# Kernel optimization log

Measured on AMD Instinct MI355X. Metric: run time of the kernel, lower is better.

Reference implementation:

```python
import jax, jax.numpy as jnp
import numpy as np

D_MODEL = 1024
NUM_HEADS = 16
HEAD_DIM = D_MODEL // NUM_HEADS


def setup_inputs() -> dict:
    key = jax.random.key(0)
    ks = jax.random.split(key, 11)
    B, S = 4, 2048
    scale = 1.0 / np.sqrt(D_MODEL)
    inp = {
        'q': jax.random.normal(ks[0], (B, S, D_MODEL), jnp.float32),
        'k': jax.random.normal(ks[1], (B, S, D_MODEL), jnp.float32),
        'v': jax.random.normal(ks[2], (B, S, D_MODEL), jnp.float32),
        'Wq': jax.random.normal(ks[3], (D_MODEL, D_MODEL), jnp.float32) * scale,
        'bq': jnp.zeros((D_MODEL,), jnp.float32),
        'Wk': jax.random.normal(ks[4], (D_MODEL, D_MODEL), jnp.float32) * scale,
        'bk': jnp.zeros((D_MODEL,), jnp.float32),
        'Wv': jax.random.normal(ks[5], (D_MODEL, D_MODEL), jnp.float32) * scale,
        'bv': jnp.zeros((D_MODEL,), jnp.float32),
        'Wo': jax.random.normal(ks[6], (D_MODEL, D_MODEL), jnp.float32) * scale,
        'bo': jnp.zeros((D_MODEL,), jnp.float32),
    }
    return inp


def _split_heads(x):
    B, S, _ = x.shape
    return x.reshape(B, S, NUM_HEADS, HEAD_DIM).transpose(0, 2, 1, 3)  # [B,H,S,Dh]


def reference(q, k, v, Wq, bq, Wk, bk, Wv, bv, Wo, bo):
    Q = _split_heads(q @ Wq.T + bq)
    K = _split_heads(k @ Wk.T + bk)
    V = _split_heads(v @ Wv.T + bv)
    scores = jnp.einsum('bhqd,bhkd->bhqk', Q, K) / jnp.sqrt(jnp.float32(HEAD_DIM))
    attn = jax.nn.softmax(scores, axis=-1)
    out = jnp.einsum('bhqk,bhkd->bhqd', attn, V)  # [B,H,S,Dh]
    B, _, S, _ = out.shape
    out = out.transpose(0, 2, 1, 3).reshape(B, S, D_MODEL)
    return out @ Wo.T + bo
```

## Files before the change

kernel.cpp:

```cpp
#include <hip/hip_runtime.h>
#include <hip/hip_bf16.h>

#define DMODEL 1024
#define NHEADS 16
#define HDIM 64

typedef __bf16 bf16_t;
typedef __bf16 bf16x8 __attribute__((ext_vector_type(8)));
typedef float  f32x4  __attribute__((ext_vector_type(4)));
typedef float  f32x16 __attribute__((ext_vector_type(16)));

__device__ __forceinline__ bf16_t f2bf(float f) {
    unsigned int u = __builtin_bit_cast(unsigned int, f);
    u += 0x7FFF + ((u >> 16) & 1);
    unsigned short h = (unsigned short)(u >> 16);
    return __builtin_bit_cast(bf16_t, h);
}

__device__ __forceinline__ unsigned cvt_pk_bf16(float lo, float hi) {
    unsigned r;
    asm("v_cvt_pk_bf16_f32 %0, %1, %2" : "=v"(r) : "v"(lo), "v"(hi));
    return r;
}

__device__ __forceinline__ void gld_lds16(const bf16_t* g, bf16_t* l) {
    __builtin_amdgcn_global_load_lds(
        (const __attribute__((address_space(1))) unsigned int*)g,
        (__attribute__((address_space(3))) unsigned int*)l, 16, 0, 0);
}

__global__ __launch_bounds__(256) void cast4(const float* __restrict__ s0,
                                             const float* __restrict__ s1,
                                             const float* __restrict__ s2,
                                             const float* __restrict__ s3,
                                             bf16_t* __restrict__ d, int n) {
    int y = blockIdx.y;
    const float* s = (y == 0) ? s0 : (y == 1) ? s1 : (y == 2) ? s2 : s3;
    bf16_t* dst = d + (size_t)y * n;
    int i = blockIdx.x * blockDim.x + threadIdx.x;
    int stride = gridDim.x * blockDim.x;
    for (int idx = i * 4; idx < n; idx += stride * 4) {
        float4 v = *reinterpret_cast<const float4*>(s + idx);
        uint2 u;
        u.x = cvt_pk_bf16(v.x, v.y);
        u.y = cvt_pk_bf16(v.z, v.w);
        *reinterpret_cast<uint2*>(dst + idx) = u;
    }
}

__global__ __launch_bounds__(256) void cast3(const float* __restrict__ q,
                                             const float* __restrict__ k,
                                             const float* __restrict__ v,
                                             bf16_t* __restrict__ qb,
                                             bf16_t* __restrict__ kb,
                                             bf16_t* __restrict__ vb, int n) {
    int z = blockIdx.y;
    const float* s = (z == 0) ? q : (z == 1) ? k : v;
    bf16_t* d = (z == 0) ? qb : (z == 1) ? kb : vb;
    int i = blockIdx.x * blockDim.x + threadIdx.x;
    int stride = gridDim.x * blockDim.x;
    for (int idx = i * 4; idx < n; idx += stride * 4) {
        float4 vv = *reinterpret_cast<const float4*>(s + idx);
        uint2 u;
        u.x = cvt_pk_bf16(vv.x, vv.y);
        u.y = cvt_pk_bf16(vv.z, vv.w);
        *reinterpret_cast<uint2*>(d + idx) = u;
    }
}

__global__ __launch_bounds__(256) void gemm_qkv(const bf16_t* __restrict__ qb,
                                                const bf16_t* __restrict__ kb,
                                                const bf16_t* __restrict__ vb,
                                                const bf16_t* __restrict__ Wall,
                                                const float* __restrict__ bq,
                                                const float* __restrict__ bk,
                                                const float* __restrict__ bv,
                                                bf16_t* __restrict__ Qp,
                                                bf16_t* __restrict__ Kp,
                                                bf16_t* __restrict__ VtG,
                                                int M, float qscale, int S) {
    __shared__ bf16_t Asmem[2][128 * 32];
    __shared__ bf16_t Bsmem[2][128 * 32];
    const int K = DMODEL, N = DMODEL;
    const int z = blockIdx.z;
    const bf16_t* Ab = (z == 0) ? qb : (z == 1) ? kb : vb;
    const bf16_t* W = Wall + (size_t)z * DMODEL * DMODEL;
    const float* bias = (z == 0) ? bq : (z == 1) ? bk : bv;
    const float scale = (z == 0) ? qscale : 1.0f;

    const int m0 = blockIdx.x * 128;
    const int n0 = blockIdx.y * 128;
    const int tid = threadIdx.x;
    const int wave = tid >> 6, lane = tid & 63;
    const int wm = wave >> 1, wn = wave & 1;
    const int lr = lane & 15, lg = lane >> 4;
    const int srow = lane >> 2, scol = (lane & 3) * 8;

    f32x4 acc[4][4];
#pragma unroll
    for (int mi = 0; mi < 4; ++mi)
#pragma unroll
        for (int ni = 0; ni < 4; ++ni) acc[mi][ni] = (f32x4){0.f, 0.f, 0.f, 0.f};

#pragma unroll
    for (int i = 0; i < 2; ++i) {
        int c = wave * 2 + i;
        gld_lds16(Ab + (size_t)(m0 + c * 16 + srow) * K + scol, &Asmem[0][c * 512]);
        gld_lds16(W + (size_t)(n0 + c * 16 + srow) * K + scol, &Bsmem[0][c * 512]);
    }
    asm volatile("s_waitcnt vmcnt(0)" ::: "memory");
    __syncthreads();

    const int nk = K / 32;
    for (int t = 0; t < nk; ++t) {
        const int cur = t & 1, nxt = cur ^ 1;
        const int ktn = (t + 1) * 32;
        if (t + 1 < nk) {
#pragma unroll
            for (int i = 0; i < 2; ++i) {
                int c = wave * 2 + i;
                gld_lds16(Ab + (size_t)(m0 + c * 16 + srow) * K + ktn + scol, &Asmem[nxt][c * 512]);
                gld_lds16(W + (size_t)(n0 + c * 16 + srow) * K + ktn + scol, &Bsmem[nxt][c * 512]);
            }
        }
        bf16x8 af[4], bfr[4];
#pragma unroll
        for (int mi = 0; mi < 4; ++mi)
            af[mi] = *reinterpret_cast<const bf16x8*>(&Asmem[cur][(wm * 64 + mi * 16 + lr) * 32 + lg * 8]);
#pragma unroll
        for (int ni = 0; ni < 4; ++ni)
            bfr[ni] = *reinterpret_cast<const bf16x8*>(&Bsmem[cur][(wn * 64 + ni * 16 + lr) * 32 + lg * 8]);
#pragma unroll
        for (int mi = 0; mi < 4; ++mi)
#pragma unroll
            for (int ni = 0; ni < 4; ++ni)
                acc[mi][ni] = __builtin_amdgcn_mfma_f32_16x16x32_bf16(af[mi], bfr[ni], acc[mi][ni], 0, 0, 0);
        asm volatile("s_waitcnt vmcnt(0)" ::: "memory");
        __syncthreads();
    }

#pragma unroll
    for (int mi = 0; mi < 4; ++mi) {
        int row = m0 + wm * 64 + mi * 16 + lg * 4;
#pragma unroll
        for (int ni = 0; ni < 4; ++ni) {
            int col = n0 + wn * 64 + ni * 16 + lr;
            float bv_ = bias[col];
            if (z == 2) {
                union { bf16_t b[4]; uint2 u; } pq;
#pragma unroll
                for (int r = 0; r < 4; ++r) pq.b[r] = f2bf(acc[mi][ni][r] + bv_);
                int b_ = row / S, s_ = row % S;
                size_t addr = (((size_t)b_ * NHEADS + (col >> 6)) * HDIM + (col & 63)) * (size_t)S + s_;
                *reinterpret_cast<uint2*>(VtG + addr) = pq.u;
            } else {
                bf16_t* Cb = (z == 0) ? Qp : Kp;
#pragma unroll
                for (int r = 0; r < 4; ++r)
                    Cb[(size_t)(row + r) * N + col] = f2bf((acc[mi][ni][r] + bv_) * scale);
            }
        }
    }
}

__global__ __launch_bounds__(256) void gemm_out(const bf16_t* __restrict__ Ab,
                                                const bf16_t* __restrict__ W,
                                                const float* __restrict__ bias,
                                                float* __restrict__ Cout,
                                                int M, int N, int K) {
    __shared__ bf16_t Asmem[2][128 * 32];
    __shared__ bf16_t Bsmem[2][128 * 32];
    const int m0 = blockIdx.x * 128;
    const int n0 = blockIdx.y * 128;
    const int tid = threadIdx.x;
    const int wave = tid >> 6, lane = tid & 63;
    const int wm = wave >> 1, wn = wave & 1;
    const int lr = lane & 15, lg = lane >> 4;
    const int srow = lane >> 2, scol = (lane & 3) * 8;

    f32x4 acc[4][4];
#pragma unroll
    for (int mi = 0; mi < 4; ++mi)
#pragma unroll
        for (int ni = 0; ni < 4; ++ni) acc[mi][ni] = (f32x4){0.f, 0.f, 0.f, 0.f};

#pragma unroll
    for (int i = 0; i < 2; ++i) {
        int c = wave * 2 + i;
        gld_lds16(Ab + (size_t)(m0 + c * 16 + srow) * K + scol, &Asmem[0][c * 512]);
        gld_lds16(W + (size_t)(n0 + c * 16 + srow) * K + scol, &Bsmem[0][c * 512]);
    }
    asm volatile("s_waitcnt vmcnt(0)" ::: "memory");
    __syncthreads();

    const int nk = K / 32;
    for (int t = 0; t < nk; ++t) {
        const int cur = t & 1, nxt = cur ^ 1;
        const int ktn = (t + 1) * 32;
        if (t + 1 < nk) {
#pragma unroll
            for (int i = 0; i < 2; ++i) {
                int c = wave * 2 + i;
                gld_lds16(Ab + (size_t)(m0 + c * 16 + srow) * K + ktn + scol, &Asmem[nxt][c * 512]);
                gld_lds16(W + (size_t)(n0 + c * 16 + srow) * K + ktn + scol, &Bsmem[nxt][c * 512]);
            }
        }
        bf16x8 af[4], bfr[4];
#pragma unroll
        for (int mi = 0; mi < 4; ++mi)
            af[mi] = *reinterpret_cast<const bf16x8*>(&Asmem[cur][(wm * 64 + mi * 16 + lr) * 32 + lg * 8]);
#pragma unroll
        for (int ni = 0; ni < 4; ++ni)
            bfr[ni] = *reinterpret_cast<const bf16x8*>(&Bsmem[cur][(wn * 64 + ni * 16 + lr) * 32 + lg * 8]);
#pragma unroll
        for (int mi = 0; mi < 4; ++mi)
#pragma unroll
            for (int ni = 0; ni < 4; ++ni)
                acc[mi][ni] = __builtin_amdgcn_mfma_f32_16x16x32_bf16(af[mi], bfr[ni], acc[mi][ni], 0, 0, 0);
        asm volatile("s_waitcnt vmcnt(0)" ::: "memory");
        __syncthreads();
    }

#pragma unroll
    for (int mi = 0; mi < 4; ++mi) {
        int row = m0 + wm * 64 + mi * 16 + lg * 4;
#pragma unroll
        for (int ni = 0; ni < 4; ++ni) {
            int col = n0 + wn * 64 + ni * 16 + lr;
            float bv = bias[col];
#pragma unroll
            for (int r = 0; r < 4; ++r)
                Cout[(size_t)(row + r) * N + col] = acc[mi][ni][r] + bv;
        }
    }
}

__global__ __launch_bounds__(256, 4) void attn_kernel(const bf16_t* __restrict__ Qp,
                                                      const bf16_t* __restrict__ Kp,
                                                      const bf16_t* __restrict__ VtG,
                                                      bf16_t* __restrict__ AO, int S) {
    __shared__ bf16_t KsA[64 * 64], KsB[64 * 64];
    __shared__ bf16_t VtA[64 * 64], VtB[64 * 64];
    const int tid = threadIdx.x;
    const int wave = tid >> 6, lane = tid & 63;
    const int ql = lane & 31;
    const int hi = lane >> 5;
    const int bh = blockIdx.y;
    const int b = bh >> 4, h = bh & 15;
    const int qt = blockIdx.x;
    const size_t base = ((size_t)b * S) * DMODEL + (size_t)h * HDIM;
    const size_t vbase = (size_t)bh * HDIM * (size_t)S;

    const int qrow = qt * 128 + wave * 32 + ql;
    bf16x8 qf[4];
#pragma unroll
    for (int kc = 0; kc < 4; ++kc)
        qf[kc] = *reinterpret_cast<const bf16x8*>(Qp + base + (size_t)qrow * DMODEL + kc * 16 + hi * 8);

    f32x16 o0{}, o1{};
    float m_r = -1e30f, l_r = 0.f;

    const int r0 = tid >> 3;
    const int swz = ((tid & 7) ^ (r0 & 7)) * 8;
    const bf16_t* Kb = Kp + base;
    const bf16_t* Vb = VtG + vbase;

    auto stageK = [&](int kv, bf16_t* buf) {
        gld_lds16(Kb + (size_t)(kv + r0) * DMODEL + swz, buf + wave * 512);
        gld_lds16(Kb + (size_t)(kv + r0 + 32) * DMODEL + swz, buf + 2048 + wave * 512);
    };
    auto stageV = [&](int kv, bf16_t* buf) {
        gld_lds16(Vb + (size_t)r0 * S + kv + swz, buf + wave * 512);
        gld_lds16(Vb + (size_t)(r0 + 32) * S + kv + swz, buf + 2048 + wave * 512);
    };

    stageK(0, KsA);
    stageV(0, VtA);
    asm volatile("s_waitcnt vmcnt(0)" ::: "memory");
    __syncthreads();

    const int NT = S / 64;
    for (int t = 0; t < NT; ++t) {
        const bf16_t* Kc = (t & 1) ? KsB : KsA;
        const bf16_t* Vc = (t & 1) ? VtB : VtA;
        bf16_t* Kn = (t & 1) ? KsA : KsB;
        bf16_t* Vn = (t & 1) ? VtA : VtB;
        if (t + 1 < NT) {
            stageK((t + 1) * 64, Kn);
            stageV((t + 1) * 64, Vn);
        }

        f32x16 s0{}, s1{};
        __builtin_amdgcn_s_setprio(1);
#pragma unroll
        for (int kc = 0; kc < 4; ++kc) {
            bf16x8 kf = *reinterpret_cast<const bf16x8*>(
                &Kc[ql * 64 + (((2 * kc + hi) ^ (ql & 7)) * 8)]);
            s0 = __builtin_amdgcn_mfma_f32_32x32x16_bf16(kf, qf[kc], s0, 0, 0, 0);
        }
#pragma unroll
        for (int kc = 0; kc < 4; ++kc) {
            bf16x8 kf = *reinterpret_cast<const bf16x8*>(
                &Kc[(32 + ql) * 64 + (((2 * kc + hi) ^ (ql & 7)) * 8)]);
            s1 = __builtin_amdgcn_mfma_f32_32x32x16_bf16(kf, qf[kc], s1, 0, 0, 0);
        }
        __builtin_amdgcn_s_setprio(0);

        float mx = s0[0];
#pragma unroll
        for (int r = 1; r < 16; ++r) mx = fmaxf(mx, s0[r]);
#pragma unroll
        for (int r = 0; r < 16; ++r) mx = fmaxf(mx, s1[r]);
        mx = fmaxf(mx, __shfl_xor(mx, 32, 64));

        if (!__all(mx <= m_r + 8.f)) {
            float mnew = fmaxf(m_r, mx);
            float fsc = __builtin_amdgcn_exp2f(m_r - mnew);
            l_r *= fsc;
            m_r = mnew;
#pragma unroll
            for (int r = 0; r < 16; ++r) { o0[r] *= fsc; o1[r] *= fsc; }
        }

        float p0[16], p1[16];
        float ssum = 0.f;
#pragma unroll
        for (int r = 0; r < 16; ++r) {
            p0[r] = __builtin_amdgcn_exp2f(s0[r] - m_r);
            p1[r] = __builtin_amdgcn_exp2f(s1[r] - m_r);
            ssum += p0[r] + p1[r];
        }
        ssum += __shfl_xor(ssum, 32, 64);
        l_r += ssum;

        unsigned w[8][2];
#pragma unroll
        for (int j = 0; j < 4; ++j) {
            w[j][0] = cvt_pk_bf16(p0[4 * j], p0[4 * j + 1]);
            w[j][1] = cvt_pk_bf16(p0[4 * j + 2], p0[4 * j + 3]);
            w[4 + j][0] = cvt_pk_bf16(p1[4 * j], p1[4 * j + 1]);
            w[4 + j][1] = cvt_pk_bf16(p1[4 * j + 2], p1[4 * j + 3]);
        }

#pragma unroll
        for (int kq = 0; kq < 4; ++kq) {
            unsigned own0 = hi ? w[2 * kq + 1][0] : w[2 * kq][0];
            unsigned own1 = hi ? w[2 * kq + 1][1] : w[2 * kq][1];
            unsigned y0 = hi ? w[2 * kq][0] : w[2 * kq + 1][0];
            unsigned y1 = hi ? w[2 * kq][1] : w[2 * kq + 1][1];
            y0 = (unsigned)__shfl_xor((int)y0, 32, 64);
            y1 = (unsigned)__shfl_xor((int)y1, 32, 64);
            union { unsigned u[4]; bf16x8 v; } pb;
            pb.u[0] = hi ? y0 : own0;
            pb.u[1] = hi ? y1 : own1;
            pb.u[2] = hi ? own0 : y0;
            pb.u[3] = hi ? own1 : y1;
            bf16x8 vf0 = *reinterpret_cast<const bf16x8*>(
                &Vc[ql * 64 + (((2 * kq + hi) ^ (ql & 7)) * 8)]);
            bf16x8 vf1 = *reinterpret_cast<const bf16x8*>(
                &Vc[(32 + ql) * 64 + (((2 * kq + hi) ^ (ql & 7)) * 8)]);
            __builtin_amdgcn_s_setprio(1);
            o0 = __builtin_amdgcn_mfma_f32_32x32x16_bf16(vf0, pb.v, o0, 0, 0, 0);
            o1 = __builtin_amdgcn_mfma_f32_32x32x16_bf16(vf1, pb.v, o1, 0, 0, 0);
            __builtin_amdgcn_s_setprio(0);
        }

        asm volatile("s_waitcnt vmcnt(0)" ::: "memory");
        __syncthreads();
    }

    float inv = 1.f / l_r;
    bf16_t* Ao = AO + base + (size_t)qrow * DMODEL;
#pragma unroll
    for (int j = 0; j < 4; ++j) {
        uint2 u0, u1;
        u0.x = cvt_pk_bf16(o0[4 * j] * inv, o0[4 * j + 1] * inv);
        u0.y = cvt_pk_bf16(o0[4 * j + 2] * inv, o0[4 * j + 3] * inv);
        *reinterpret_cast<uint2*>(Ao + 8 * j + 4 * hi) = u0;
        u1.x = cvt_pk_bf16(o1[4 * j] * inv, o1[4 * j + 1] * inv);
        u1.y = cvt_pk_bf16(o1[4 * j + 2] * inv, o1[4 * j + 3] * inv);
        *reinterpret_cast<uint2*>(Ao + 32 + 8 * j + 4 * hi) = u1;
    }
}

extern "C" void kernel_launch(void* const* d_in, const int* in_sizes, int n_in,
                              void* d_out, int out_size, void* d_ws, size_t ws_size,
                              hipStream_t stream) {
    const float* q  = (const float*)d_in[0];
    const float* k  = (const float*)d_in[1];
    const float* v  = (const float*)d_in[2];
    const float* Wq = (const float*)d_in[3];
    const float* bq = (const float*)d_in[4];
    const float* Wk = (const float*)d_in[5];
    const float* bk = (const float*)d_in[6];
    const float* Wv = (const float*)d_in[7];
    const float* bv = (const float*)d_in[8];
    const float* Wo = (const float*)d_in[9];
    const float* bo = (const float*)d_in[10];

    const int M = in_sizes[0] / DMODEL;
    const int S = 2048;
    const int B = M / S;

    bf16_t* ws  = (bf16_t*)d_ws;
    const size_t WSZ = (size_t)DMODEL * DMODEL;
    const size_t MSZ = (size_t)M * DMODEL;
    bf16_t* Wqb = ws;
    bf16_t* Wob = Wqb + 3 * WSZ;
    bf16_t* Qp  = Wob + WSZ;
    bf16_t* Kp  = Qp + MSZ;
    bf16_t* VtG = Kp + MSZ;
    bf16_t* shX = VtG + MSZ;
    bf16_t* qb  = (bf16_t*)d_out;
    bf16_t* kb  = qb + MSZ;
    bf16_t* vb  = shX;
    bf16_t* AO  = shX;

    cast4<<<dim3(1024, 4), 256, 0, stream>>>(Wq, Wk, Wv, Wo, ws, DMODEL * DMODEL);
    cast3<<<dim3(2048, 3), 256, 0, stream>>>(q, k, v, qb, kb, vb, M * DMODEL);

    const float qscale = 0.125f * 1.44269504088896f;
    gemm_qkv<<<dim3(M / 128, DMODEL / 128, 3), 256, 0, stream>>>(
        qb, kb, vb, Wqb, bq, bk, bv, Qp, Kp, VtG, M, qscale, S);

    attn_kernel<<<dim3(S / 128, B * NHEADS), 256, 0, stream>>>(Qp, Kp, VtG, AO, S);

    gemm_out<<<dim3(M / 128, DMODEL / 128), 256, 0, stream>>>(
        AO, Wob, bo, (float*)d_out, M, DMODEL, DMODEL);
}
```

Measured before the change: 239.5 us.

## Process two query tiles per attention block and merge cast kernels

Each attention block now handles 256 query rows, with each wave carrying two independent 32-row query groups. Every K and V tile staged in LDS feeds twice as many MFMAs, which halves K/V global traffic and interleaves two independent softmax/MFMA chains. The main loop is manually unrolled by two to drop the buffer-select branches. Occupancy bound drops to 2 blocks per CU because of the extra accumulator registers, and the grid is halved to 512 blocks. The weight and activation cast kernels are also merged into one launch.

```diff
diff --git a/kernel.cpp b/kernel.cpp
--- a/kernel.cpp
+++ b/kernel.cpp
@@ -29,34 +29,29 @@
         (__attribute__((address_space(3))) unsigned int*)l, 16, 0, 0);
 }
 
-__global__ __launch_bounds__(256) void cast4(const float* __restrict__ s0,
-                                             const float* __restrict__ s1,
-                                             const float* __restrict__ s2,
-                                             const float* __restrict__ s3,
-                                             bf16_t* __restrict__ d, int n) {
-    int y = blockIdx.y;
-    const float* s = (y == 0) ? s0 : (y == 1) ? s1 : (y == 2) ? s2 : s3;
-    bf16_t* dst = d + (size_t)y * n;
-    int i = blockIdx.x * blockDim.x + threadIdx.x;
-    int stride = gridDim.x * blockDim.x;
-    for (int idx = i * 4; idx < n; idx += stride * 4) {
-        float4 v = *reinterpret_cast<const float4*>(s + idx);
-        uint2 u;
-        u.x = cvt_pk_bf16(v.x, v.y);
-        u.y = cvt_pk_bf16(v.z, v.w);
-        *reinterpret_cast<uint2*>(dst + idx) = u;
-    }
-}
-
-__global__ __launch_bounds__(256) void cast3(const float* __restrict__ q,
-                                             const float* __restrict__ k,
-                                             const float* __restrict__ v,
-                                             bf16_t* __restrict__ qb,
-                                             bf16_t* __restrict__ kb,
-                                             bf16_t* __restrict__ vb, int n) {
-    int z = blockIdx.y;
-    const float* s = (z == 0) ? q : (z == 1) ? k : v;
-    bf16_t* d = (z == 0) ? qb : (z == 1) ? kb : vb;
+__global__ __launch_bounds__(256) void cast_all(const float* __restrict__ Wq,
+                                                const float* __restrict__ Wk,
+                                                const float* __restrict__ Wv,
+                                                const float* __restrict__ Wo,
+                                                const float* __restrict__ q,
+                                                const float* __restrict__ k,
+                                                const float* __restrict__ v,
+                                                bf16_t* __restrict__ Wall,
+                                                bf16_t* __restrict__ qb,
+                                                bf16_t* __restrict__ kb,
+                                                bf16_t* __restrict__ vb,
+                                                int nw, int na) {
+    const int y = blockIdx.y;
+    const float* s;
+    bf16_t* d;
+    int n;
+    if (y == 0)      { s = Wq; d = Wall;               n = nw; }
+    else if (y == 1) { s = Wk; d = Wall + (size_t)nw;  n = nw; }
+    else if (y == 2) { s = Wv; d = Wall + 2 * (size_t)nw; n = nw; }
+    else if (y == 3) { s = Wo; d = Wall + 3 * (size_t)nw; n = nw; }
+    else if (y == 4) { s = q;  d = qb; n = na; }
+    else if (y == 5) { s = k;  d = kb; n = na; }
+    else             { s = v;  d = vb; n = na; }
     int i = blockIdx.x * blockDim.x + threadIdx.x;
     int stride = gridDim.x * blockDim.x;
     for (int idx = i * 4; idx < n; idx += stride * 4) {
@@ -235,7 +230,7 @@
     }
 }
 
-__global__ __launch_bounds__(256, 4) void attn_kernel(const bf16_t* __restrict__ Qp,
+__global__ __launch_bounds__(256, 2) void attn_kernel(const bf16_t* __restrict__ Qp,
                                                       const bf16_t* __restrict__ Kp,
                                                       const bf16_t* __restrict__ VtG,
                                                       bf16_t* __restrict__ AO, int S) {
@@ -251,14 +246,18 @@
     const size_t base = ((size_t)b * S) * DMODEL + (size_t)h * HDIM;
     const size_t vbase = (size_t)bh * HDIM * (size_t)S;
 
-    const int qrow = qt * 128 + wave * 32 + ql;
-    bf16x8 qf[4];
-#pragma unroll
-    for (int kc = 0; kc < 4; ++kc)
-        qf[kc] = *reinterpret_cast<const bf16x8*>(Qp + base + (size_t)qrow * DMODEL + kc * 16 + hi * 8);
-
-    f32x16 o0{}, o1{};
-    float m_r = -1e30f, l_r = 0.f;
+    const int qrowA = qt * 256 + wave * 32 + ql;
+    const int qrowB = qrowA + 128;
+    bf16x8 qfA[4], qfB[4];
+#pragma unroll
+    for (int kc = 0; kc < 4; ++kc) {
+        qfA[kc] = *reinterpret_cast<const bf16x8*>(Qp + base + (size_t)qrowA * DMODEL + kc * 16 + hi * 8);
+        qfB[kc] = *reinterpret_cast<const bf16x8*>(Qp + base + (size_t)qrowB * DMODEL + kc * 16 + hi * 8);
+    }
+
+    f32x16 oA0{}, oA1{}, oB0{}, oB1{};
+    float mA = -1e30f, lA = 0.f;
+    float mB = -1e30f, lB = 0.f;
 
     const int r0 = tid >> 3;
     const int swz = ((tid & 7) ^ (r0 & 7)) * 8;
@@ -274,45 +273,14 @@
         gld_lds16(Vb + (size_t)(r0 + 32) * S + kv + swz, buf + 2048 + wave * 512);
     };
 
-    stageK(0, KsA);
-    stageV(0, VtA);
-    asm volatile("s_waitcnt vmcnt(0)" ::: "memory");
-    __syncthreads();
-
-    const int NT = S / 64;
-    for (int t = 0; t < NT; ++t) {
-        const bf16_t* Kc = (t & 1) ? KsB : KsA;
-        const bf16_t* Vc = (t & 1) ? VtB : VtA;
-        bf16_t* Kn = (t & 1) ? KsA : KsB;
-        bf16_t* Vn = (t & 1) ? VtA : VtB;
-        if (t + 1 < NT) {
-            stageK((t + 1) * 64, Kn);
-            stageV((t + 1) * 64, Vn);
-        }
-
-        f32x16 s0{}, s1{};
-        __builtin_amdgcn_s_setprio(1);
-#pragma unroll
-        for (int kc = 0; kc < 4; ++kc) {
-            bf16x8 kf = *reinterpret_cast<const bf16x8*>(
-                &Kc[ql * 64 + (((2 * kc + hi) ^ (ql & 7)) * 8)]);
-            s0 = __builtin_amdgcn_mfma_f32_32x32x16_bf16(kf, qf[kc], s0, 0, 0, 0);
-        }
-#pragma unroll
-        for (int kc = 0; kc < 4; ++kc) {
-            bf16x8 kf = *reinterpret_cast<const bf16x8*>(
-                &Kc[(32 + ql) * 64 + (((2 * kc + hi) ^ (ql & 7)) * 8)]);
-            s1 = __builtin_amdgcn_mfma_f32_32x32x16_bf16(kf, qf[kc], s1, 0, 0, 0);
-        }
-        __builtin_amdgcn_s_setprio(0);
-
+    auto softmax_pack = [&](f32x16& s0, f32x16& s1, f32x16& o0, f32x16& o1,
+                            float& m_r, float& l_r, unsigned (&w)[8][2]) {
         float mx = s0[0];
 #pragma unroll
         for (int r = 1; r < 16; ++r) mx = fmaxf(mx, s0[r]);
 #pragma unroll
         for (int r = 0; r < 16; ++r) mx = fmaxf(mx, s1[r]);
         mx = fmaxf(mx, __shfl_xor(mx, 32, 64));
-
         if (!__all(mx <= m_r + 8.f)) {
             float mnew = fmaxf(m_r, mx);
             float fsc = __builtin_amdgcn_exp2f(m_r - mnew);
@@ -321,7 +289,6 @@
 #pragma unroll
             for (int r = 0; r < 16; ++r) { o0[r] *= fsc; o1[r] *= fsc; }
         }
-
         float p0[16], p1[16];
         float ssum = 0.f;
 #pragma unroll
@@ -332,8 +299,6 @@
         }
         ssum += __shfl_xor(ssum, 32, 64);
         l_r += ssum;
-
-        unsigned w[8][2];
 #pragma unroll
         for (int j = 0; j < 4; ++j) {
             w[j][0] = cvt_pk_bf16(p0[4 * j], p0[4 * j + 1]);
@@ -341,45 +306,104 @@
             w[4 + j][0] = cvt_pk_bf16(p1[4 * j], p1[4 * j + 1]);
             w[4 + j][1] = cvt_pk_bf16(p1[4 * j + 2], p1[4 * j + 3]);
         }
+    };
+
+    auto build_pb = [&](unsigned (&w)[8][2], int kq) {
+        unsigned own0 = hi ? w[2 * kq + 1][0] : w[2 * kq][0];
+        unsigned own1 = hi ? w[2 * kq + 1][1] : w[2 * kq][1];
+        unsigned y0 = hi ? w[2 * kq][0] : w[2 * kq + 1][0];
+        unsigned y1 = hi ? w[2 * kq][1] : w[2 * kq + 1][1];
+        y0 = (unsigned)__shfl_xor((int)y0, 32, 64);
+        y1 = (unsigned)__shfl_xor((int)y1, 32, 64);
+        union { unsigned u[4]; bf16x8 v; } pb;
+        pb.u[0] = hi ? y0 : own0;
+        pb.u[1] = hi ? y1 : own1;
+        pb.u[2] = hi ? own0 : y0;
+        pb.u[3] = hi ? own1 : y1;
+        return pb.v;
+    };
+
+    const int NT = S / 64;
+    auto tile = [&](const bf16_t* Kc, const bf16_t* Vc, bf16_t* Kn, bf16_t* Vn, int t) {
+        if (t + 1 < NT) {
+            stageK((t + 1) * 64, Kn);
+            stageV((t + 1) * 64, Vn);
+        }
+        f32x16 sA0{}, sA1{}, sB0{}, sB1{};
+        __builtin_amdgcn_s_setprio(1);
+#pragma unroll
+        for (int kc = 0; kc < 4; ++kc) {
+            bf16x8 kf0 = *reinterpret_cast<const bf16x8*>(
+                &Kc[ql * 64 + (((2 * kc + hi) ^ (ql & 7)) * 8)]);
+            sA0 = __builtin_amdgcn_mfma_f32_32x32x16_bf16(kf0, qfA[kc], sA0, 0, 0, 0);
+            sB0 = __builtin_amdgcn_mfma_f32_32x32x16_bf16(kf0, qfB[kc], sB0, 0, 0, 0);
+            bf16x8 kf1 = *reinterpret_cast<const bf16x8*>(
+                &Kc[(32 + ql) * 64 + (((2 * kc + hi) ^ (ql & 7)) * 8)]);
+            sA1 = __builtin_amdgcn_mfma_f32_32x32x16_bf16(kf1, qfA[kc], sA1, 0, 0, 0);
+            sB1 = __builtin_amdgcn_mfma_f32_32x32x16_bf16(kf1, qfB[kc], sB1, 0, 0, 0);
+        }
+        __builtin_amdgcn_s_setprio(0);
+
+        unsigned wA[8][2], wB[8][2];
+        softmax_pack(sA0, sA1, oA0, oA1, mA, lA, wA);
+        softmax_pack(sB0, sB1, oB0, oB1, mB, lB, wB);
 
 #pragma unroll
         for (int kq = 0; kq < 4; ++kq) {
-            unsigned own0 = hi ? w[2 * kq + 1][0] : w[2 * kq][0];
-            unsigned own1 = hi ? w[2 * kq + 1][1] : w[2 * kq][1];
-            unsigned y0 = hi ? w[2 * kq][0] : w[2 * kq + 1][0];
-            unsigned y1 = hi ? w[2 * kq][1] : w[2 * kq + 1][1];
-            y0 = (unsigned)__shfl_xor((int)y0, 32, 64);
-            y1 = (unsigned)__shfl_xor((int)y1, 32, 64);
-            union { unsigned u[4]; bf16x8 v; } pb;
-            pb.u[0] = hi ? y0 : own0;
-            pb.u[1] = hi ? y1 : own1;
-            pb.u[2] = hi ? own0 : y0;
-            pb.u[3] = hi ? own1 : y1;
+            bf16x8 pbA = build_pb(wA, kq);
+            bf16x8 pbB = build_pb(wB, kq);
             bf16x8 vf0 = *reinterpret_cast<const bf16x8*>(
                 &Vc[ql * 64 + (((2 * kq + hi) ^ (ql & 7)) * 8)]);
             bf16x8 vf1 = *reinterpret_cast<const bf16x8*>(
                 &Vc[(32 + ql) * 64 + (((2 * kq + hi) ^ (ql & 7)) * 8)]);
             __builtin_amdgcn_s_setprio(1);
-            o0 = __builtin_amdgcn_mfma_f32_32x32x16_bf16(vf0, pb.v, o0, 0, 0, 0);
-            o1 = __builtin_amdgcn_mfma_f32_32x32x16_bf16(vf1, pb.v, o1, 0, 0, 0);
+            oA0 = __builtin_amdgcn_mfma_f32_32x32x16_bf16(vf0, pbA, oA0, 0, 0, 0);
+            oA1 = __builtin_amdgcn_mfma_f32_32x32x16_bf16(vf1, pbA, oA1, 0, 0, 0);
+            oB0 = __builtin_amdgcn_mfma_f32_32x32x16_bf16(vf0, pbB, oB0, 0, 0, 0);
+            oB1 = __builtin_amdgcn_mfma_f32_32x32x16_bf16(vf1, pbB, oB1, 0, 0, 0);
             __builtin_amdgcn_s_setprio(0);
         }
-
         asm volatile("s_waitcnt vmcnt(0)" ::: "memory");
         __syncthreads();
-    }
-
-    float inv = 1.f / l_r;
-    bf16_t* Ao = AO + base + (size_t)qrow * DMODEL;
-#pragma unroll
-    for (int j = 0; j < 4; ++j) {
-        uint2 u0, u1;
-        u0.x = cvt_pk_bf16(o0[4 * j] * inv, o0[4 * j + 1] * inv);
-        u0.y = cvt_pk_bf16(o0[4 * j + 2] * inv, o0[4 * j + 3] * inv);
-        *reinterpret_cast<uint2*>(Ao + 8 * j + 4 * hi) = u0;
-        u1.x = cvt_pk_bf16(o1[4 * j] * inv, o1[4 * j + 1] * inv);
-        u1.y = cvt_pk_bf16(o1[4 * j + 2] * inv, o1[4 * j + 3] * inv);
-        *reinterpret_cast<uint2*>(Ao + 32 + 8 * j + 4 * hi) = u1;
+    };
+
+    stageK(0, KsA);
+    stageV(0, VtA);
+    asm volatile("s_waitcnt vmcnt(0)" ::: "memory");
+    __syncthreads();
+
+    for (int t = 0; t < NT; t += 2) {
+        tile(KsA, VtA, KsB, VtB, t);
+        tile(KsB, VtB, KsA, VtA, t + 1);
+    }
+
+    {
+        float inv = 1.f / lA;
+        bf16_t* Ao = AO + base + (size_t)qrowA * DMODEL;
+#pragma unroll
+        for (int j = 0; j < 4; ++j) {
+            uint2 u0, u1;
+            u0.x = cvt_pk_bf16(oA0[4 * j] * inv, oA0[4 * j + 1] * inv);
+            u0.y = cvt_pk_bf16(oA0[4 * j + 2] * inv, oA0[4 * j + 3] * inv);
+            *reinterpret_cast<uint2*>(Ao + 8 * j + 4 * hi) = u0;
+            u1.x = cvt_pk_bf16(oA1[4 * j] * inv, oA1[4 * j + 1] * inv);
+            u1.y = cvt_pk_bf16(oA1[4 * j + 2] * inv, oA1[4 * j + 3] * inv);
+            *reinterpret_cast<uint2*>(Ao + 32 + 8 * j + 4 * hi) = u1;
+        }
+    }
+    {
+        float inv = 1.f / lB;
+        bf16_t* Ao = AO + base + (size_t)qrowB * DMODEL;
+#pragma unroll
+        for (int j = 0; j < 4; ++j) {
+            uint2 u0, u1;
+            u0.x = cvt_pk_bf16(oB0[4 * j] * inv, oB0[4 * j + 1] * inv);
+            u0.y = cvt_pk_bf16(oB0[4 * j + 2] * inv, oB0[4 * j + 3] * inv);
+            *reinterpret_cast<uint2*>(Ao + 8 * j + 4 * hi) = u0;
+            u1.x = cvt_pk_bf16(oB1[4 * j] * inv, oB1[4 * j + 1] * inv);
+            u1.y = cvt_pk_bf16(oB1[4 * j + 2] * inv, oB1[4 * j + 3] * inv);
+            *reinterpret_cast<uint2*>(Ao + 32 + 8 * j + 4 * hi) = u1;
+        }
     }
 }
 
@@ -416,14 +440,15 @@
     bf16_t* vb  = shX;
     bf16_t* AO  = shX;
 
-    cast4<<<dim3(1024, 4), 256, 0, stream>>>(Wq, Wk, Wv, Wo, ws, DMODEL * DMODEL);
-    cast3<<<dim3(2048, 3), 256, 0, stream>>>(q, k, v, qb, kb, vb, M * DMODEL);
+    cast_all<<<dim3(2048, 7), 256, 0, stream>>>(Wq, Wk, Wv, Wo, q, k, v,
+                                                ws, qb, kb, vb,
+                                                DMODEL * DMODEL, M * DMODEL);
 
     const float qscale = 0.125f * 1.44269504088896f;
     gemm_qkv<<<dim3(M / 128, DMODEL / 128, 3), 256, 0, stream>>>(
         qb, kb, vb, Wqb, bq, bk, bv, Qp, Kp, VtG, M, qscale, S);
 
-    attn_kernel<<<dim3(S / 128, B * NHEADS), 256, 0, stream>>>(Qp, Kp, VtG, AO, S);
+    attn_kernel<<<dim3(S / 256, B * NHEADS), 256, 0, stream>>>(Qp, Kp, VtG, AO, S);
 
     gemm_out<<<dim3(M / 128, DMODEL / 128), 256, 0, stream>>>(
         AO, Wob, bo, (float*)d_out, M, DMODEL, DMODEL);
```

After: 230.8 us. 1.04x faster.

## Widen attention KV tile to 128, swap grid axes, merge cast kernels

Applied to the files above, without the earlier changes.

The attention kernel now processes 128 keys per iteration instead of 64, with larger double-buffered K and V tiles in LDS and a loop unrolled by two to drop buffer-select logic. This halves the number of barrier and online-softmax rescale steps, at the cost of more registers and LDS per block, so the occupancy hint drops to 2 blocks. The grid axes are swapped so blocks on the same head run close together, which may improve L2 reuse of K and V. The two fp32-to-bf16 cast kernels are merged into one launch.

```diff
diff --git a/kernel.cpp b/kernel.cpp
--- a/kernel.cpp
+++ b/kernel.cpp
@@ -29,34 +29,29 @@
         (__attribute__((address_space(3))) unsigned int*)l, 16, 0, 0);
 }
 
-__global__ __launch_bounds__(256) void cast4(const float* __restrict__ s0,
-                                             const float* __restrict__ s1,
-                                             const float* __restrict__ s2,
-                                             const float* __restrict__ s3,
-                                             bf16_t* __restrict__ d, int n) {
-    int y = blockIdx.y;
-    const float* s = (y == 0) ? s0 : (y == 1) ? s1 : (y == 2) ? s2 : s3;
-    bf16_t* dst = d + (size_t)y * n;
-    int i = blockIdx.x * blockDim.x + threadIdx.x;
-    int stride = gridDim.x * blockDim.x;
-    for (int idx = i * 4; idx < n; idx += stride * 4) {
-        float4 v = *reinterpret_cast<const float4*>(s + idx);
-        uint2 u;
-        u.x = cvt_pk_bf16(v.x, v.y);
-        u.y = cvt_pk_bf16(v.z, v.w);
-        *reinterpret_cast<uint2*>(dst + idx) = u;
-    }
-}
-
-__global__ __launch_bounds__(256) void cast3(const float* __restrict__ q,
-                                             const float* __restrict__ k,
-                                             const float* __restrict__ v,
-                                             bf16_t* __restrict__ qb,
-                                             bf16_t* __restrict__ kb,
-                                             bf16_t* __restrict__ vb, int n) {
-    int z = blockIdx.y;
-    const float* s = (z == 0) ? q : (z == 1) ? k : v;
-    bf16_t* d = (z == 0) ? qb : (z == 1) ? kb : vb;
+__global__ __launch_bounds__(256) void cast_all(const float* __restrict__ Wq,
+                                                const float* __restrict__ Wk,
+                                                const float* __restrict__ Wv,
+                                                const float* __restrict__ Wo,
+                                                const float* __restrict__ q,
+                                                const float* __restrict__ k,
+                                                const float* __restrict__ v,
+                                                bf16_t* __restrict__ Wall,
+                                                bf16_t* __restrict__ qb,
+                                                bf16_t* __restrict__ kb,
+                                                bf16_t* __restrict__ vb,
+                                                int nw, int na) {
+    const int y = blockIdx.y;
+    const float* s;
+    bf16_t* d;
+    int n;
+    if (y == 0)      { s = Wq; d = Wall;               n = nw; }
+    else if (y == 1) { s = Wk; d = Wall + (size_t)nw;  n = nw; }
+    else if (y == 2) { s = Wv; d = Wall + 2 * (size_t)nw; n = nw; }
+    else if (y == 3) { s = Wo; d = Wall + 3 * (size_t)nw; n = nw; }
+    else if (y == 4) { s = q;  d = qb; n = na; }
+    else if (y == 5) { s = k;  d = kb; n = na; }
+    else             { s = v;  d = vb; n = na; }
     int i = blockIdx.x * blockDim.x + threadIdx.x;
     int stride = gridDim.x * blockDim.x;
     for (int idx = i * 4; idx < n; idx += stride * 4) {
@@ -235,19 +230,19 @@
     }
 }
 
-__global__ __launch_bounds__(256, 4) void attn_kernel(const bf16_t* __restrict__ Qp,
+__global__ __launch_bounds__(256, 2) void attn_kernel(const bf16_t* __restrict__ Qp,
                                                       const bf16_t* __restrict__ Kp,
                                                       const bf16_t* __restrict__ VtG,
                                                       bf16_t* __restrict__ AO, int S) {
-    __shared__ bf16_t KsA[64 * 64], KsB[64 * 64];
-    __shared__ bf16_t VtA[64 * 64], VtB[64 * 64];
+    __shared__ bf16_t KsA[128 * 64], KsB[128 * 64];
+    __shared__ bf16_t VtA[64 * 128], VtB[64 * 128];
     const int tid = threadIdx.x;
     const int wave = tid >> 6, lane = tid & 63;
     const int ql = lane & 31;
     const int hi = lane >> 5;
-    const int bh = blockIdx.y;
+    const int bh = blockIdx.x;
     const int b = bh >> 4, h = bh & 15;
-    const int qt = blockIdx.x;
+    const int qt = blockIdx.y;
     const size_t base = ((size_t)b * S) * DMODEL + (size_t)h * HDIM;
     const size_t vbase = (size_t)bh * HDIM * (size_t)S;
 
@@ -260,57 +255,51 @@
     f32x16 o0{}, o1{};
     float m_r = -1e30f, l_r = 0.f;
 
-    const int r0 = tid >> 3;
-    const int swz = ((tid & 7) ^ (r0 & 7)) * 8;
+    const int r0k = tid >> 3;
+    const int swzk = ((tid & 7) ^ (r0k & 7)) * 8;
+    const int r0v = tid >> 4;
+    const int swzv = ((tid & 15) ^ (r0v & 7)) * 8;
     const bf16_t* Kb = Kp + base;
     const bf16_t* Vb = VtG + vbase;
 
     auto stageK = [&](int kv, bf16_t* buf) {
-        gld_lds16(Kb + (size_t)(kv + r0) * DMODEL + swz, buf + wave * 512);
-        gld_lds16(Kb + (size_t)(kv + r0 + 32) * DMODEL + swz, buf + 2048 + wave * 512);
+#pragma unroll
+        for (int i = 0; i < 4; ++i)
+            gld_lds16(Kb + (size_t)(kv + r0k + 32 * i) * DMODEL + swzk,
+                      buf + i * 2048 + wave * 512);
     };
     auto stageV = [&](int kv, bf16_t* buf) {
-        gld_lds16(Vb + (size_t)r0 * S + kv + swz, buf + wave * 512);
-        gld_lds16(Vb + (size_t)(r0 + 32) * S + kv + swz, buf + 2048 + wave * 512);
+#pragma unroll
+        for (int i = 0; i < 4; ++i)
+            gld_lds16(Vb + (size_t)(r0v + 16 * i) * S + kv + swzv,
+                      buf + i * 2048 + wave * 512);
     };
 
-    stageK(0, KsA);
-    stageV(0, VtA);
-    asm volatile("s_waitcnt vmcnt(0)" ::: "memory");
-    __syncthreads();
-
-    const int NT = S / 64;
-    for (int t = 0; t < NT; ++t) {
-        const bf16_t* Kc = (t & 1) ? KsB : KsA;
-        const bf16_t* Vc = (t & 1) ? VtB : VtA;
-        bf16_t* Kn = (t & 1) ? KsA : KsB;
-        bf16_t* Vn = (t & 1) ? VtA : VtB;
+    const int NT = S / 128;
+    auto tile = [&](const bf16_t* Kc, const bf16_t* Vc, bf16_t* Kn, bf16_t* Vn, int t) {
         if (t + 1 < NT) {
-            stageK((t + 1) * 64, Kn);
-            stageV((t + 1) * 64, Vn);
-        }
-
-        f32x16 s0{}, s1{};
+            stageK((t + 1) * 128, Kn);
+            stageV((t + 1) * 128, Vn);
+        }
+
+        f32x16 s[4] = {};
         __builtin_amdgcn_s_setprio(1);
 #pragma unroll
-        for (int kc = 0; kc < 4; ++kc) {
-            bf16x8 kf = *reinterpret_cast<const bf16x8*>(
-                &Kc[ql * 64 + (((2 * kc + hi) ^ (ql & 7)) * 8)]);
-            s0 = __builtin_amdgcn_mfma_f32_32x32x16_bf16(kf, qf[kc], s0, 0, 0, 0);
-        }
-#pragma unroll
-        for (int kc = 0; kc < 4; ++kc) {
-            bf16x8 kf = *reinterpret_cast<const bf16x8*>(
-                &Kc[(32 + ql) * 64 + (((2 * kc + hi) ^ (ql & 7)) * 8)]);
-            s1 = __builtin_amdgcn_mfma_f32_32x32x16_bf16(kf, qf[kc], s1, 0, 0, 0);
+        for (int g = 0; g < 4; ++g) {
+#pragma unroll
+            for (int kc = 0; kc < 4; ++kc) {
+                bf16x8 kf = *reinterpret_cast<const bf16x8*>(
+                    &Kc[(32 * g + ql) * 64 + (((2 * kc + hi) ^ (ql & 7)) * 8)]);
+                s[g] = __builtin_amdgcn_mfma_f32_32x32x16_bf16(kf, qf[kc], s[g], 0, 0, 0);
+            }
         }
         __builtin_amdgcn_s_setprio(0);
 
-        float mx = s0[0];
-#pragma unroll
-        for (int r = 1; r < 16; ++r) mx = fmaxf(mx, s0[r]);
-#pragma unroll
-        for (int r = 0; r < 16; ++r) mx = fmaxf(mx, s1[r]);
+        float mx = s[0][0];
+#pragma unroll
+        for (int g = 0; g < 4; ++g)
+#pragma unroll
+            for (int r = 0; r < 16; ++r) mx = fmaxf(mx, s[g][r]);
         mx = fmaxf(mx, __shfl_xor(mx, 32, 64));
 
         if (!__all(mx <= m_r + 8.f)) {
@@ -322,32 +311,33 @@
             for (int r = 0; r < 16; ++r) { o0[r] *= fsc; o1[r] *= fsc; }
         }
 
-        float p0[16], p1[16];
         float ssum = 0.f;
 #pragma unroll
-        for (int r = 0; r < 16; ++r) {
-            p0[r] = __builtin_amdgcn_exp2f(s0[r] - m_r);
-            p1[r] = __builtin_amdgcn_exp2f(s1[r] - m_r);
-            ssum += p0[r] + p1[r];
-        }
+        for (int g = 0; g < 4; ++g)
+#pragma unroll
+            for (int r = 0; r < 16; ++r) {
+                s[g][r] = __builtin_amdgcn_exp2f(s[g][r] - m_r);
+                ssum += s[g][r];
+            }
         ssum += __shfl_xor(ssum, 32, 64);
         l_r += ssum;
 
-        unsigned w[8][2];
-#pragma unroll
-        for (int j = 0; j < 4; ++j) {
-            w[j][0] = cvt_pk_bf16(p0[4 * j], p0[4 * j + 1]);
-            w[j][1] = cvt_pk_bf16(p0[4 * j + 2], p0[4 * j + 3]);
-            w[4 + j][0] = cvt_pk_bf16(p1[4 * j], p1[4 * j + 1]);
-            w[4 + j][1] = cvt_pk_bf16(p1[4 * j + 2], p1[4 * j + 3]);
-        }
-
-#pragma unroll
-        for (int kq = 0; kq < 4; ++kq) {
-            unsigned own0 = hi ? w[2 * kq + 1][0] : w[2 * kq][0];
-            unsigned own1 = hi ? w[2 * kq + 1][1] : w[2 * kq][1];
-            unsigned y0 = hi ? w[2 * kq][0] : w[2 * kq + 1][0];
-            unsigned y1 = hi ? w[2 * kq][1] : w[2 * kq + 1][1];
+        unsigned w[16][2];
+#pragma unroll
+        for (int g = 0; g < 4; ++g)
+#pragma unroll
+            for (int j = 0; j < 4; ++j) {
+                w[4 * g + j][0] = cvt_pk_bf16(s[g][4 * j], s[g][4 * j + 1]);
+                w[4 * g + j][1] = cvt_pk_bf16(s[g][4 * j + 2], s[g][4 * j + 3]);
+            }
+
+#pragma unroll
+        for (int kq = 0; kq < 8; ++kq) {
+            const int wb = 2 * kq;
+            unsigned own0 = hi ? w[wb + 1][0] : w[wb][0];
+            unsigned own1 = hi ? w[wb + 1][1] : w[wb][1];
+            unsigned y0 = hi ? w[wb][0] : w[wb + 1][0];
+            unsigned y1 = hi ? w[wb][1] : w[wb + 1][1];
             y0 = (unsigned)__shfl_xor((int)y0, 32, 64);
             y1 = (unsigned)__shfl_xor((int)y1, 32, 64);
             union { unsigned u[4]; bf16x8 v; } pb;
@@ -355,10 +345,11 @@
             pb.u[1] = hi ? y1 : own1;
             pb.u[2] = hi ? own0 : y0;
             pb.u[3] = hi ? own1 : y1;
+            const int c = 2 * kq + hi;
             bf16x8 vf0 = *reinterpret_cast<const bf16x8*>(
-                &Vc[ql * 64 + (((2 * kq + hi) ^ (ql & 7)) * 8)]);
+                &Vc[ql * 128 + ((c ^ (ql & 7)) * 8)]);
             bf16x8 vf1 = *reinterpret_cast<const bf16x8*>(
-                &Vc[(32 + ql) * 64 + (((2 * kq + hi) ^ (ql & 7)) * 8)]);
+                &Vc[(32 + ql) * 128 + ((c ^ (ql & 7)) * 8)]);
             __builtin_amdgcn_s_setprio(1);
             o0 = __builtin_amdgcn_mfma_f32_32x32x16_bf16(vf0, pb.v, o0, 0, 0, 0);
             o1 = __builtin_amdgcn_mfma_f32_32x32x16_bf16(vf1, pb.v, o1, 0, 0, 0);
@@ -367,6 +358,16 @@
 
         asm volatile("s_waitcnt vmcnt(0)" ::: "memory");
         __syncthreads();
+    };
+
+    stageK(0, KsA);
+    stageV(0, VtA);
+    asm volatile("s_waitcnt vmcnt(0)" ::: "memory");
+    __syncthreads();
+
+    for (int t = 0; t < NT; t += 2) {
+        tile(KsA, VtA, KsB, VtB, t);
+        tile(KsB, VtB, KsA, VtA, t + 1);
     }
 
     float inv = 1.f / l_r;
@@ -416,14 +417,15 @@
     bf16_t* vb  = shX;
     bf16_t* AO  = shX;
 
-    cast4<<<dim3(1024, 4), 256, 0, stream>>>(Wq, Wk, Wv, Wo, ws, DMODEL * DMODEL);
-    cast3<<<dim3(2048, 3), 256, 0, stream>>>(q, k, v, qb, kb, vb, M * DMODEL);
+    cast_all<<<dim3(2048, 7), 256, 0, stream>>>(Wq, Wk, Wv, Wo, q, k, v,
+                                                ws, qb, kb, vb,
+                                                DMODEL * DMODEL, M * DMODEL);
 
     const float qscale = 0.125f * 1.44269504088896f;
     gemm_qkv<<<dim3(M / 128, DMODEL / 128, 3), 256, 0, stream>>>(
         qb, kb, vb, Wqb, bq, bk, bv, Qp, Kp, VtG, M, qscale, S);
 
-    attn_kernel<<<dim3(S / 128, B * NHEADS), 256, 0, stream>>>(Qp, Kp, VtG, AO, S);
+    attn_kernel<<<dim3(B * NHEADS, S / 128), 256, 0, stream>>>(Qp, Kp, VtG, AO, S);
 
     gemm_out<<<dim3(M / 128, DMODEL / 128), 256, 0, stream>>>(
         AO, Wob, bo, (float*)d_out, M, DMODEL, DMODEL);
```

Measured after the change: 235.4 us. Within noise of the previous version (-1.7%).
